# Kernel tuning notes

Measured on AMD Instinct MI355X. Metric: run time of the kernel, lower is better.

The kernel has to match this reference:

```python
import jax, jax.numpy as jnp
from jax import lax
import numpy as np

BNF = float((1.0 + 1e-5) ** -0.5)  # eval-mode BatchNorm with fresh init (mean=0,var=1,gamma=1,beta=0)
DN = ('NCHW', 'OIHW', 'NCHW')


def conv(x, w, b, stride=1, pad=1):
    y = lax.conv_general_dilated(x, w, (stride, stride), [(pad, pad), (pad, pad)], dimension_numbers=DN)
    return y + b[None, :, None, None]


def conv_t(x, w, b, stride=2, pad=1):
    # w in PyTorch ConvTranspose2d layout [Cin, Cout, kh, kw]
    wf = jnp.flip(w, (2, 3)).transpose(1, 0, 2, 3)  # -> [Cout, Cin, kh, kw]
    p = w.shape[2] - 1 - pad
    y = lax.conv_general_dilated(x, wf, (1, 1), [(p, p), (p, p)], lhs_dilation=(stride, stride), dimension_numbers=DN)
    return y + b[None, :, None, None]


def res_block(x, c1w, c1b, c2w, c2b, scw, scb, stride):
    sc = conv(x, scw, scb, stride, 0) * BNF
    h = jax.nn.relu(conv(x, c1w, c1b, stride, 1) * BNF)
    h = conv(h, c2w, c2b, 1, 1) * BNF
    return jax.nn.relu(h + sc)


def setup_inputs() -> dict:
    key = jax.random.key(0)
    ks = jax.random.split(key, 32)
    s = 0.05
    d = {}
    d['x'] = jax.random.normal(ks[0], (4, 1, 320, 320), jnp.float32)
    # encoder (scale_idx=3, scale_channels=512, embedding_dim=256)
    d['w0'] = jax.random.normal(ks[1], (128, 1, 3, 3)) * s;   d['b0'] = jnp.zeros((128,))
    d['a_c1w'] = jax.random.normal(ks[2], (256, 128, 3, 3)) * s; d['a_c1b'] = jnp.zeros((256,))
    d['a_c2w'] = jax.random.normal(ks[3], (256, 256, 3, 3)) * s; d['a_c2b'] = jnp.zeros((256,))
    d['a_scw'] = jax.random.normal(ks[4], (256, 128, 1, 1)) * s; d['a_scb'] = jnp.zeros((256,))
    d['b_c1w'] = jax.random.normal(ks[5], (512, 256, 3, 3)) * s; d['b_c1b'] = jnp.zeros((512,))
    d['b_c2w'] = jax.random.normal(ks[6], (512, 512, 3, 3)) * s; d['b_c2b'] = jnp.zeros((512,))
    d['b_scw'] = jax.random.normal(ks[7], (512, 256, 1, 1)) * s; d['b_scb'] = jnp.zeros((512,))
    d['ew'] = jax.random.normal(ks[8], (256, 512, 1, 1)) * s;    d['eb'] = jnp.zeros((256,))
    # codebook: uniform(-1/K, 1/K)
    d['codebook'] = jax.random.uniform(ks[9], (1024, 256), jnp.float32, -1.0 / 1024, 1.0 / 1024)
    # decoder
    d['d0w'] = jax.random.normal(ks[10], (512, 256, 1, 1)) * s;  d['d0b'] = jnp.zeros((512,))
    d['dt1w'] = jax.random.normal(ks[11], (512, 256, 4, 4)) * s; d['dt1b'] = jnp.zeros((256,))
    d['dt2w'] = jax.random.normal(ks[12], (256, 128, 4, 4)) * s; d['dt2b'] = jnp.zeros((128,))
    d['dow'] = jax.random.normal(ks[13], (1, 128, 3, 3)) * s;    d['dob'] = jnp.zeros((1,))
    return d


def reference(x, w0, b0, a_c1w, a_c1b, a_c2w, a_c2b, a_scw, a_scb,
              b_c1w, b_c1b, b_c2w, b_c2b, b_scw, b_scb, ew, eb, codebook,
              d0w, d0b, dt1w, dt1b, dt2w, dt2b, dow, dob):
    B = x.shape[0]
    # ---- encoder ----
    h = jax.nn.relu(conv(x, w0, b0, 1, 1) * BNF)                      # [B,128,320,320]
    h = res_block(h, a_c1w, a_c1b, a_c2w, a_c2b, a_scw, a_scb, 2)     # [B,256,160,160]
    h = res_block(h, b_c1w, b_c1b, b_c2w, b_c2b, b_scw, b_scb, 2)     # [B,512,80,80]
    z = conv(h, ew, eb, 1, 0) * BNF                                   # [B,256,80,80]
    # ---- vector quantize (faithful: flatten NCHW directly, D == embedding_dim) ----
    D = codebook.shape[1]
    flat = z.reshape(-1, D)                                           # [B*H*W, 256]
    dist = (jnp.sum(flat * flat, 1, keepdims=True)
            + jnp.sum(codebook * codebook, 1)
            - 2.0 * flat @ codebook.T)                                # [N, 1024]
    idx = jnp.argmin(dist, axis=1)                                    # [N]
    quant = codebook[idx].reshape(z.shape)
    zq = z + lax.stop_gradient(quant - z)                             # straight-through
    indices = idx.reshape(B, z.shape[2], z.shape[3]).astype(jnp.int32)
    # ---- decoder ----
    g = jax.nn.relu(conv(zq, d0w, d0b, 1, 0) * BNF)                   # [B,512,80,80]
    g = jax.nn.relu(conv_t(g, dt1w, dt1b) * BNF)                      # [B,256,160,160]
    g = jax.nn.relu(conv_t(g, dt2w, dt2b) * BNF)                      # [B,128,320,320]
    recon = jax.nn.sigmoid(conv(g, dow, dob, 1, 1))                   # [B,1,320,320]
    return recon, zq, indices
```

## Files before the change

### kernel.cpp

```cpp
#include <hip/hip_runtime.h>
#include <hip/hip_bf16.h>
#include <math.h>


static constexpr float kBNF = 0.9999950000374997f;

typedef short short8 __attribute__((ext_vector_type(8)));
typedef _Float16 half8 __attribute__((ext_vector_type(8)));
typedef float f32x4 __attribute__((ext_vector_type(4)));

__global__ __launch_bounds__(320) void conv0_k(const float* __restrict__ x,
                                               const float* __restrict__ w,
                                               const float* __restrict__ b,
                                               float* __restrict__ out) {
  const int H = 320, W = 320, OC = 128;
  int oy = blockIdx.x;
  int tx = threadIdx.x;
  __shared__ float in_s[3][W + 2];
  __shared__ float w_s[128 * 9];
  __shared__ float b_s[128];
  for (int e = tx; e < 3 * (W + 2); e += 320) {
    int r = e / (W + 2), c = e % (W + 2);
    int iy = oy + r - 1, ix = c - 1;
    float v = 0.f;
    if (iy >= 0 && iy < H && ix >= 0 && ix < W) v = x[iy * W + ix];
    in_s[r][c] = v;
  }
  for (int e = tx; e < 128 * 9; e += 320) w_s[e] = w[e];
  for (int e = tx; e < 128; e += 320) b_s[e] = b[e];
  __syncthreads();
  float iv[9];
#pragma unroll
  for (int r = 0; r < 3; ++r)
#pragma unroll
    for (int c = 0; c < 3; ++c) iv[r * 3 + c] = in_s[r][tx + c];
  for (int oc = 0; oc < OC; ++oc) {
    float acc = 0.f;
#pragma unroll
    for (int t = 0; t < 9; ++t) acc = fmaf(w_s[oc * 9 + t], iv[t], acc);
    float v32 = __fadd_rn(acc, b_s[oc]);
    v32 = __fmul_rn(v32, kBNF);
    out[(oc * H + oy) * W + tx] = fmaxf(v32, 0.f);
  }
}

__global__ __launch_bounds__(256) void prep_w3h_k(const float* __restrict__ w,
                                                  _Float16* __restrict__ wh,
                                                  int IC, int OC) {
  int i = blockIdx.x * 256 + threadIdx.x;
  int total = 2 * 9 * IC * OC;
  if (i >= total) return;
  int e = i & 7;
  int lane = (i >> 3) & 63;
  int rest = i >> 9;
  int ktiles = IC >> 5;
  int kT = rest % ktiles;
  int rest2 = rest / ktiles;
  int OCt = OC >> 4;
  int ocT = rest2 % OCt;
  int rest3 = rest2 / OCt;
  int tap = rest3 % 9;
  int split = rest3 / 9;
  int m = lane & 15, k = ((lane >> 4) << 3) + e;
  int oc = ocT * 16 + m, ic = kT * 32 + k;
  float v = w[((size_t)oc * IC + ic) * 9 + tap];
  _Float16 hi = (_Float16)v;
  wh[i] = (split == 0) ? hi : (_Float16)(v - (float)hi);
}

__global__ __launch_bounds__(256) void conv3s1_mfma_k(
    const float* __restrict__ in, const _Float16* __restrict__ wh,
    const float* __restrict__ bias, const float* __restrict__ skip,
    float* __restrict__ out, int IC, int HW_, int OC) {
  __shared__ __align__(16) _Float16 ldsH[3 * 20 * 40];
  __shared__ __align__(16) _Float16 ldsL[3 * 20 * 40];
  int t = threadIdx.x;
  int wv = t >> 6, l = t & 63;
  int px0 = blockIdx.x * 16;
  int oy = blockIdx.y;
  int ocT = blockIdx.z * 4 + wv;
  const int ktiles = IC >> 5;
  const int OCt = OC >> 4;
  int n = l & 15, koff = (l >> 4) * 8;
  f32x4 acc = {0.f, 0.f, 0.f, 0.f};
  const half8* wh8 = reinterpret_cast<const half8*>(wh);
  for (int kT = 0; kT < ktiles; ++kT) {
    __syncthreads();
    for (int e = t; e < 1728; e += 256) {
      int xi = e % 18;
      int rem = e / 18;
      int ic = rem & 31, r = rem >> 5;
      int iy = oy - 1 + r;
      int ix = px0 - 1 + xi;
      float v = 0.f;
      if (iy >= 0 && iy < HW_ && ix >= 0 && ix < HW_)
        v = in[((size_t)(kT * 32 + ic) * HW_ + iy) * HW_ + ix];
      _Float16 hi = (_Float16)v;
      ldsH[(r * 20 + xi) * 40 + ic] = hi;
      ldsL[(r * 20 + xi) * 40 + ic] = (_Float16)(v - (float)hi);
    }
    __syncthreads();
#pragma unroll
    for (int ky = 0; ky < 3; ++ky) {
#pragma unroll
      for (int kx = 0; kx < 3; ++kx) {
        int tap = ky * 3 + kx;
        half8 AH = wh8[(((tap)*OCt + ocT) * ktiles + kT) * 64 + l];
        half8 AL = wh8[(((9 + tap) * OCt + ocT) * ktiles + kT) * 64 + l];
        half8 BH = *reinterpret_cast<const half8*>(&ldsH[(ky * 20 + n + kx) * 40 + koff]);
        half8 BL = *reinterpret_cast<const half8*>(&ldsL[(ky * 20 + n + kx) * 40 + koff]);
        acc = __builtin_amdgcn_mfma_f32_16x16x32_f16(AH, BH, acc, 0, 0, 0);
        acc = __builtin_amdgcn_mfma_f32_16x16x32_f16(AH, BL, acc, 0, 0, 0);
        acc = __builtin_amdgcn_mfma_f32_16x16x32_f16(AL, BH, acc, 0, 0, 0);
      }
    }
  }
  int oc0 = ocT * 16 + ((l >> 4) << 2);
  int ox = px0 + n;
#pragma unroll
  for (int r = 0; r < 4; ++r) {
    int oc = oc0 + r;
    float bv = bias[oc];
    size_t idx = ((size_t)oc * HW_ + oy) * HW_ + ox;
    float v32 = __fadd_rn(acc[r], bv);
    v32 = __fmul_rn(v32, kBNF);
    v32 = __fadd_rn(v32, skip[idx]);
    out[idx] = fmaxf(v32, 0.f);
  }
}

__global__ __launch_bounds__(256) void conv3s2_mfma_k(
    const float* __restrict__ in, const _Float16* __restrict__ wh,
    const float* __restrict__ bias, float* __restrict__ out,
    int IC, int IH, int IW, int OC, int OH, int OW) {
  __shared__ __align__(16) _Float16 ldsEH[3 * 17 * 40];
  __shared__ __align__(16) _Float16 ldsEL[3 * 17 * 40];
  __shared__ __align__(16) _Float16 ldsOH[3 * 16 * 40];
  __shared__ __align__(16) _Float16 ldsOL[3 * 16 * 40];
  int t = threadIdx.x;
  int wv = t >> 6, l = t & 63;
  int px0 = blockIdx.x * 16;
  int oy = blockIdx.y;
  int ocT = blockIdx.z * 4 + wv;
  const int ktiles = IC >> 5;
  const int OCt = OC >> 4;
  int n = l & 15, koff = (l >> 4) * 8;
  f32x4 acc = {0.f, 0.f, 0.f, 0.f};
  const half8* wh8 = reinterpret_cast<const half8*>(wh);
  for (int kT = 0; kT < ktiles; ++kT) {
    __syncthreads();
    for (int e = t; e < 3168; e += 256) {
      int ic = e & 31;
      int rem = e >> 5;
      int xi = rem % 33, ky = rem / 33;
      int iy = oy * 2 - 1 + ky;
      int ix = px0 * 2 - 1 + xi;
      float v = 0.f;
      if (iy >= 0 && iy < IH && ix >= 0 && ix < IW)
        v = in[((size_t)(kT * 32 + ic) * IH + iy) * IW + ix];
      _Float16 hi = (_Float16)v;
      _Float16 lo = (_Float16)(v - (float)hi);
      int hrow = xi >> 1;
      if (xi & 1) {
        ldsOH[(ky * 16 + hrow) * 40 + ic] = hi;
        ldsOL[(ky * 16 + hrow) * 40 + ic] = lo;
      } else {
        ldsEH[(ky * 17 + hrow) * 40 + ic] = hi;
        ldsEL[(ky * 17 + hrow) * 40 + ic] = lo;
      }
    }
    __syncthreads();
#pragma unroll
    for (int ky = 0; ky < 3; ++ky) {
#pragma unroll
      for (int kx = 0; kx < 3; ++kx) {
        int tap = ky * 3 + kx;
        half8 AH = wh8[(((tap)*OCt + ocT) * ktiles + kT) * 64 + l];
        half8 AL = wh8[(((9 + tap) * OCt + ocT) * ktiles + kT) * 64 + l];
        half8 BH, BL;
        if (kx == 0) {
          BH = *reinterpret_cast<const half8*>(&ldsEH[(ky * 17 + n) * 40 + koff]);
          BL = *reinterpret_cast<const half8*>(&ldsEL[(ky * 17 + n) * 40 + koff]);
        } else if (kx == 1) {
          BH = *reinterpret_cast<const half8*>(&ldsOH[(ky * 16 + n) * 40 + koff]);
          BL = *reinterpret_cast<const half8*>(&ldsOL[(ky * 16 + n) * 40 + koff]);
        } else {
          BH = *reinterpret_cast<const half8*>(&ldsEH[(ky * 17 + n + 1) * 40 + koff]);
          BL = *reinterpret_cast<const half8*>(&ldsEL[(ky * 17 + n + 1) * 40 + koff]);
        }
        acc = __builtin_amdgcn_mfma_f32_16x16x32_f16(AH, BH, acc, 0, 0, 0);
        acc = __builtin_amdgcn_mfma_f32_16x16x32_f16(AH, BL, acc, 0, 0, 0);
        acc = __builtin_amdgcn_mfma_f32_16x16x32_f16(AL, BH, acc, 0, 0, 0);
      }
    }
  }
  int oc0 = ocT * 16 + ((l >> 4) << 2);
  int ox = px0 + n;
#pragma unroll
  for (int r = 0; r < 4; ++r) {
    int oc = oc0 + r;
    float bv = bias[oc];
    size_t idx = ((size_t)oc * OH + oy) * OW + ox;
    float v32 = __fadd_rn(acc[r], bv);
    v32 = __fmul_rn(v32, kBNF);
    out[idx] = fmaxf(v32, 0.f);
  }
}

template <int S, bool RELU>
__global__ __launch_bounds__(256) void conv1x1_k(
    const float* __restrict__ in, const float* __restrict__ w,
    const float* __restrict__ bias, float* __restrict__ out,
    int IC, int IH, int IW, int OC, int OH, int OW) {
  __shared__ float in_s[16][64];
  __shared__ float w_s[16][64];
  const int P = OH * OW;
  int t = threadIdx.x;
  int p0 = blockIdx.x * 64;
  int oc0 = blockIdx.y * 64;
  int oc4 = (t >> 4) * 4, px4 = (t & 15) * 4;
  float acc[4][4] = {};
  for (int ic0 = 0; ic0 < IC; ic0 += 16) {
    __syncthreads();
    {
      int e = t;
#pragma unroll
      for (int k = 0; k < 4; ++k, e += 256) {
        int icr = e >> 6, pxr = e & 63;
        int p = p0 + pxr;
        float v = 0.f;
        if (p < P) {
          int oy = p / OW, ox = p % OW;
          v = in[((ic0 + icr) * IH + oy * S) * IW + ox * S];
        }
        in_s[icr][pxr] = v;
      }
      e = t;
#pragma unroll
      for (int k = 0; k < 4; ++k, e += 256) {
        int icr = e >> 6, ocr = e & 63;
        w_s[icr][ocr] = w[(oc0 + ocr) * IC + ic0 + icr];
      }
    }
    __syncthreads();
#pragma unroll
    for (int icr = 0; icr < 16; ++icr) {
      float4 iv = *reinterpret_cast<const float4*>(&in_s[icr][px4]);
      float4 wv = *reinterpret_cast<const float4*>(&w_s[icr][oc4]);
      const float* ip = (const float*)&iv;
      const float* wp = (const float*)&wv;
#pragma unroll
      for (int o = 0; o < 4; ++o)
#pragma unroll
        for (int p = 0; p < 4; ++p)
          acc[o][p] = fmaf(wp[o], ip[p], acc[o][p]);
    }
  }
  int p = p0 + px4;
  if (p < P) {
    int oy = p / OW, ox = p % OW;
#pragma unroll
    for (int o = 0; o < 4; ++o) {
      int oc = oc0 + oc4 + o;
      float bv = bias[oc];
      float4 rv;
      float* rp = (float*)&rv;
#pragma unroll
      for (int pp = 0; pp < 4; ++pp) {
        float v32 = __fadd_rn(acc[o][pp], bv);
        v32 = __fmul_rn(v32, kBNF);
        if (RELU) v32 = fmaxf(v32, 0.f);
        rp[pp] = v32;
      }
      *reinterpret_cast<float4*>(&out[((size_t)oc * OH + oy) * OW + ox]) = rv;
    }
  }
}

__global__ __launch_bounds__(256) void prep_wb_k(const float* __restrict__ w,
                                                 __hip_bfloat16* __restrict__ wb,
                                                 int IC, int OC) {
  int i = blockIdx.x * 256 + threadIdx.x;
  int total = 16 * IC * OC;
  if (i >= total) return;
  int per_cfg = IC * OC;
  int cfg = i / per_cfg;
  int r = i - cfg * per_cfg;
  int ktiles = IC >> 5;
  int ocT = r / (ktiles * 512);
  int r2 = r - ocT * (ktiles * 512);
  int kT = r2 >> 9;
  int f = r2 & 511;
  int lane = f >> 3, e = f & 7;
  int m = lane & 15, kk = ((lane >> 4) << 3) + e;
  int oc = ocT * 16 + m, ic = kT * 32 + kk;
  int kyb = cfg >> 3, ty = (cfg >> 2) & 1, kx = cfg & 3;
  int ky = kyb + 2 * ty;
  wb[i] = __float2bfloat16(w[((size_t)ic * OC + oc) * 16 + ky * 4 + kx]);
}

__global__ __launch_bounds__(256) void convt_mfma_k(
    const float* __restrict__ in, const __hip_bfloat16* __restrict__ wb,
    const float* __restrict__ bias, float* __restrict__ out,
    int IC, int IH, int IW, int OC, int OH, int OW) {
  __shared__ __align__(16) __hip_bfloat16 lds[2 * 18 * 40];
  int t = threadIdx.x;
  int wv = t >> 6, l = t & 63;
  int ox0 = blockIdx.x * 32;
  int oy = blockIdx.y;
  int oc0w = blockIdx.z * 64 + wv * 16;
  int kyb = (oy & 1) ? 0 : 1;
  int hb = ox0 >> 1;
  int iy0n = oy + 1 - kyb;
  int iy0 = iy0n >> 1;
  bool ok0 = (iy0 < IH);
  int iy1n = oy + 1 - kyb - 2;
  int iy1 = iy1n >> 1;
  bool ok1 = (iy1n >= 0) && (iy1 < IH);
  f32x4 accE = {0.f, 0.f, 0.f, 0.f};
  f32x4 accO = {0.f, 0.f, 0.f, 0.f};
  const int ktiles = IC >> 5;
  int n = l & 15, koff = (l >> 4) * 8;
  const short8* wb8 = reinterpret_cast<const short8*>(wb);
  int ocT = oc0w >> 4;
  const int OCt = OC >> 4;
  for (int kT = 0; kT < ktiles; ++kT) {
    __syncthreads();
    for (int e = t; e < 1152; e += 256) {
      int ic = e / 36;
      int r = e - ic * 36;
      int ty = r / 18, xi = r - ty * 18;
      int ix = hb - 1 + xi;
      int iy = ty ? iy1 : iy0;
      bool ok = ty ? ok1 : ok0;
      float v = 0.f;
      if (ok && ix >= 0 && ix < IW)
        v = in[((size_t)(kT * 32 + ic) * IH + iy) * IW + ix];
      lds[(ty * 18 + xi) * 40 + ic] = __float2bfloat16(v);
    }
    __syncthreads();
#pragma unroll
    for (int ty = 0; ty < 2; ++ty) {
      short8 A0 = wb8[((((kyb * 2 + ty) * 4 + 0) * OCt + ocT) * ktiles + kT) * 64 + l];
      short8 A1 = wb8[((((kyb * 2 + ty) * 4 + 1) * OCt + ocT) * ktiles + kT) * 64 + l];
      short8 A2 = wb8[((((kyb * 2 + ty) * 4 + 2) * OCt + ocT) * ktiles + kT) * 64 + l];
      short8 A3 = wb8[((((kyb * 2 + ty) * 4 + 3) * OCt + ocT) * ktiles + kT) * 64 + l];
      short8 b0 = *reinterpret_cast<const short8*>(&lds[(ty * 18 + 0 + n) * 40 + koff]);
      short8 b1 = *reinterpret_cast<const short8*>(&lds[(ty * 18 + 1 + n) * 40 + koff]);
      short8 b2 = *reinterpret_cast<const short8*>(&lds[(ty * 18 + 2 + n) * 40 + koff]);
      accE = __builtin_amdgcn_mfma_f32_16x16x32_bf16(A1, b1, accE, 0, 0, 0);
      accE = __builtin_amdgcn_mfma_f32_16x16x32_bf16(A3, b0, accE, 0, 0, 0);
      accO = __builtin_amdgcn_mfma_f32_16x16x32_bf16(A0, b2, accO, 0, 0, 0);
      accO = __builtin_amdgcn_mfma_f32_16x16x32_bf16(A2, b1, accO, 0, 0, 0);
    }
  }
  int ocr0 = oc0w + ((l >> 4) << 2);
  int oxE = ox0 + 2 * n;
  int oxO = ox0 + 1 + 2 * n;
#pragma unroll
  for (int r = 0; r < 4; ++r) {
    float bv = bias[ocr0 + r];
    size_t rowbase = ((size_t)(ocr0 + r) * OH + oy) * OW;
    out[rowbase + oxE] = fmaxf((accE[r] + bv) * kBNF, 0.f);
    out[rowbase + oxO] = fmaxf((accO[r] + bv) * kBNF, 0.f);
  }
}

__global__ __launch_bounds__(320) void dow_k(const float* __restrict__ in,
                                             const float* __restrict__ w,
                                             const float* __restrict__ bias,
                                             float* __restrict__ out) {
  const int H = 320, W = 320, IC = 128;
  int oy = blockIdx.x;
  int tx = threadIdx.x;
  __shared__ float in_s[4][3][W + 2];
  __shared__ float w_s[IC * 9];
  for (int e = tx; e < IC * 9; e += 320) w_s[e] = w[e];
  float acc = 0.f;
  for (int ic0 = 0; ic0 < IC; ic0 += 4) {
    __syncthreads();
    for (int e = tx; e < 4 * 3 * (W + 2); e += 320) {
      int icr = e / (3 * (W + 2));
      int rem = e - icr * (3 * (W + 2));
      int r = rem / (W + 2), c = rem - r * (W + 2);
      int iy = oy + r - 1, ix = c - 1;
      float v = 0.f;
      if (iy >= 0 && iy < H && ix >= 0 && ix < W)
        v = in[((ic0 + icr) * H + iy) * W + ix];
      in_s[icr][r][c] = v;
    }
    __syncthreads();
#pragma unroll
    for (int icr = 0; icr < 4; ++icr)
#pragma unroll
      for (int r = 0; r < 3; ++r)
#pragma unroll
        for (int c = 0; c < 3; ++c)
          acc = fmaf(w_s[(ic0 + icr) * 9 + r * 3 + c], in_s[icr][r][tx + c], acc);
  }
  acc += bias[0];
  out[oy * W + tx] = 1.f / (1.f + expf(-acc));
}

__global__ __launch_bounds__(256) void cbprep_np(const float* __restrict__ cb,
                                                 float* __restrict__ c2f) {
  int e = blockIdx.x, t = threadIdx.x;
  __shared__ float a[256];
  a[t] = cb[e * 256 + t];
  __syncthreads();
  if (t == 0) {
    float tot = 0.f;
    for (int h = 0; h < 2; ++h) {
      const float* p = a + h * 128;
      float r[8];
#pragma unroll
      for (int j = 0; j < 8; ++j) r[j] = __fmul_rn(p[j], p[j]);
      for (int i = 8; i < 128; i += 8)
#pragma unroll
        for (int j = 0; j < 8; ++j) r[j] = __fadd_rn(r[j], __fmul_rn(p[i + j], p[i + j]));
      float s = __fadd_rn(__fadd_rn(__fadd_rn(r[0], r[1]), __fadd_rn(r[2], r[3])),
                          __fadd_rn(__fadd_rn(r[4], r[5]), __fadd_rn(r[6], r[7])));
      tot = (h == 0) ? s : __fadd_rn(tot, s);
    }
    c2f[e] = tot;
  }
}

__global__ __launch_bounds__(256) void vq_ref_k(const float* __restrict__ z,
                                                const float* __restrict__ cb,
                                                const float* __restrict__ c2f,
                                                float* __restrict__ zq_out,
                                                float* __restrict__ idx_out) {
  int n0 = blockIdx.x * 4;
  int t = threadIdx.x;
  __shared__ float f[4][256];
  __shared__ float dist[4][1024];
  __shared__ float rr[4][2][8];
  __shared__ float f2s[4];
  __shared__ int bestIdx[4];
  for (int e = t; e < 1024; e += 256) {
    int r = e >> 8, c = e & 255;
    f[r][c] = z[(size_t)(n0 + r) * 256 + c];
  }
  __syncthreads();
  if (t < 64) {
    int row = t >> 4, hh = (t >> 3) & 1, j = t & 7;
    const float* p = f[row] + hh * 128;
    float r = __fmul_rn(p[j], p[j]);
    for (int i = 8; i < 128; i += 8) r = __fadd_rn(r, __fmul_rn(p[i + j], p[i + j]));
    rr[row][hh][j] = r;
  }
  __syncthreads();
  if (t < 4) {
    float s0 = __fadd_rn(__fadd_rn(__fadd_rn(rr[t][0][0], rr[t][0][1]), __fadd_rn(rr[t][0][2], rr[t][0][3])),
                         __fadd_rn(__fadd_rn(rr[t][0][4], rr[t][0][5]), __fadd_rn(rr[t][0][6], rr[t][0][7])));
    float s1 = __fadd_rn(__fadd_rn(__fadd_rn(rr[t][1][0], rr[t][1][1]), __fadd_rn(rr[t][1][2], rr[t][1][3])),
                         __fadd_rn(__fadd_rn(rr[t][1][4], rr[t][1][5]), __fadd_rn(rr[t][1][6], rr[t][1][7])));
    f2s[t] = __fadd_rn(s0, s1);
  }
  __syncthreads();
  for (int e = t; e < 1024; e += 256) {
    const float4* cbe = reinterpret_cast<const float4*>(cb + (size_t)e * 256);
    double d0 = 0.0, d1 = 0.0, d2 = 0.0, d3 = 0.0;
    for (int d = 0; d < 64; ++d) {
      float4 c4 = cbe[d];
      float4 f0 = *reinterpret_cast<const float4*>(&f[0][d * 4]);
      float4 f1 = *reinterpret_cast<const float4*>(&f[1][d * 4]);
      float4 f2v = *reinterpret_cast<const float4*>(&f[2][d * 4]);
      float4 f3 = *reinterpret_cast<const float4*>(&f[3][d * 4]);
      d0 = fma((double)f0.x, (double)c4.x, d0); d0 = fma((double)f0.y, (double)c4.y, d0);
      d0 = fma((double)f0.z, (double)c4.z, d0); d0 = fma((double)f0.w, (double)c4.w, d0);
      d1 = fma((double)f1.x, (double)c4.x, d1); d1 = fma((double)f1.y, (double)c4.y, d1);
      d1 = fma((double)f1.z, (double)c4.z, d1); d1 = fma((double)f1.w, (double)c4.w, d1);
      d2 = fma((double)f2v.x, (double)c4.x, d2); d2 = fma((double)f2v.y, (double)c4.y, d2);
      d2 = fma((double)f2v.z, (double)c4.z, d2); d2 = fma((double)f2v.w, (double)c4.w, d2);
      d3 = fma((double)f3.x, (double)c4.x, d3); d3 = fma((double)f3.y, (double)c4.y, d3);
      d3 = fma((double)f3.z, (double)c4.z, d3); d3 = fma((double)f3.w, (double)c4.w, d3);
    }
    float c2e = c2f[e];
    dist[0][e] = __fsub_rn(__fadd_rn(f2s[0], c2e), __fmul_rn(2.f, (float)d0));
    dist[1][e] = __fsub_rn(__fadd_rn(f2s[1], c2e), __fmul_rn(2.f, (float)d1));
    dist[2][e] = __fsub_rn(__fadd_rn(f2s[2], c2e), __fmul_rn(2.f, (float)d2));
    dist[3][e] = __fsub_rn(__fadd_rn(f2s[3], c2e), __fmul_rn(2.f, (float)d3));
  }
  __syncthreads();
  {
    int row = t >> 6, l = t & 63;
    float bv = dist[row][l];
    int bi = l;
    for (int e = l + 64; e < 1024; e += 64) {
      float v = dist[row][e];
      if (v < bv) { bv = v; bi = e; }
    }
#pragma unroll
    for (int m = 1; m < 64; m <<= 1) {
      float ov = __shfl_xor(bv, m, 64);
      int oi = __shfl_xor(bi, m, 64);
      if (ov < bv || (ov == bv && oi < bi)) { bv = ov; bi = oi; }
    }
    if (l == 0) {
      bestIdx[row] = bi;
      idx_out[n0 + row] = (float)bi;
    }
  }
  __syncthreads();
#pragma unroll
  for (int r = 0; r < 4; ++r)
    zq_out[(size_t)(n0 + r) * 256 + t] = cb[(size_t)bestIdx[r] * 256 + t];
}

extern "C" void kernel_launch(void* const* d_in, const int* in_sizes, int n_in,
                              void* d_out, int out_size, void* d_ws, size_t ws_size,
                              hipStream_t stream) {
  const float* x = (const float*)d_in[0];
  const float* w0 = (const float*)d_in[1];
  const float* b0 = (const float*)d_in[2];
  const float* a_c1w = (const float*)d_in[3];
  const float* a_c1b = (const float*)d_in[4];
  const float* a_c2w = (const float*)d_in[5];
  const float* a_c2b = (const float*)d_in[6];
  const float* a_scw = (const float*)d_in[7];
  const float* a_scb = (const float*)d_in[8];
  const float* b_c1w = (const float*)d_in[9];
  const float* b_c1b = (const float*)d_in[10];
  const float* b_c2w = (const float*)d_in[11];
  const float* b_c2b = (const float*)d_in[12];
  const float* b_scw = (const float*)d_in[13];
  const float* b_scb = (const float*)d_in[14];
  const float* ew = (const float*)d_in[15];
  const float* eb = (const float*)d_in[16];
  const float* cb = (const float*)d_in[17];
  const float* d0w = (const float*)d_in[18];
  const float* d0b = (const float*)d_in[19];
  const float* dt1w = (const float*)d_in[20];
  const float* dt1b = (const float*)d_in[21];
  const float* dt2w = (const float*)d_in[22];
  const float* dt2b = (const float*)d_in[23];
  const float* doww = (const float*)d_in[24];
  const float* dob = (const float*)d_in[25];

  float* ws = (float*)d_ws;
  float* A = ws;
  float* Bf = ws + 13107200;
  float* Cf = ws + 19660800;
  float* c2f = ws + 26214400;
  _Float16* wh_ac1 = (_Float16*)(void*)Cf;
  _Float16* wh_bc1 = (_Float16*)(void*)(Bf + 3300000);
  _Float16* wh_ac2 = (_Float16*)(void*)(A + 6600000);
  _Float16* wh_bc2 = (_Float16*)(void*)(A + 3300000);
  __hip_bfloat16* wb_dt1 = (__hip_bfloat16*)(void*)A;
  __hip_bfloat16* wb_dt2 = (__hip_bfloat16*)(void*)(Bf + 3400000);

  float* outf = (float*)d_out;
  float* recon = outf;
  float* zq = outf + 409600;
  float* idxo = zq + 6553600;

  cbprep_np<<<1024, 256, 0, stream>>>(cb, c2f);

  for (int b = 0; b < 4; ++b) {
    const float* xb = x + (size_t)b * 102400;
    float* zqb = zq + (size_t)b * 1638400;
    float* idxb = idxo + (size_t)b * 6400;
    float* reconb = recon + (size_t)b * 102400;

    conv0_k<<<320, 320, 0, stream>>>(xb, w0, b0, A);
    prep_w3h_k<<<2304, 256, 0, stream>>>(a_c1w, wh_ac1, 128, 256);
    conv3s2_mfma_k<<<dim3(10, 160, 4), 256, 0, stream>>>(
        A, wh_ac1, a_c1b, Bf, 128, 320, 320, 256, 160, 160);
    conv1x1_k<2, false><<<dim3(400, 4), 256, 0, stream>>>(
        A, a_scw, a_scb, Cf, 128, 320, 320, 256, 160, 160);
    prep_w3h_k<<<4608, 256, 0, stream>>>(a_c2w, wh_ac2, 256, 256);
    conv3s1_mfma_k<<<dim3(10, 160, 4), 256, 0, stream>>>(
        Bf, wh_ac2, a_c2b, Cf, A, 256, 160, 256);
    prep_w3h_k<<<9216, 256, 0, stream>>>(b_c1w, wh_bc1, 256, 512);
    conv3s2_mfma_k<<<dim3(5, 80, 8), 256, 0, stream>>>(
        A, wh_bc1, b_c1b, Bf, 256, 160, 160, 512, 80, 80);
    conv1x1_k<2, false><<<dim3(100, 8), 256, 0, stream>>>(
        A, b_scw, b_scb, Cf, 256, 160, 160, 512, 80, 80);
    prep_w3h_k<<<18432, 256, 0, stream>>>(b_c2w, wh_bc2, 512, 512);
    conv3s1_mfma_k<<<dim3(5, 80, 8), 256, 0, stream>>>(
        Bf, wh_bc2, b_c2b, Cf, A, 512, 80, 512);
    conv1x1_k<1, false><<<dim3(100, 4), 256, 0, stream>>>(
        A, ew, eb, Cf, 512, 80, 80, 256, 80, 80);
    vq_ref_k<<<1600, 256, 0, stream>>>(Cf, cb, c2f, zqb, idxb);
    prep_wb_k<<<8192, 256, 0, stream>>>(dt1w, wb_dt1, 512, 256);
    prep_wb_k<<<2048, 256, 0, stream>>>(dt2w, wb_dt2, 256, 128);
    conv1x1_k<1, true><<<dim3(100, 8), 256, 0, stream>>>(
        zqb, d0w, d0b, Bf, 256, 80, 80, 512, 80, 80);
    convt_mfma_k<<<dim3(5, 160, 4), 256, 0, stream>>>(
        Bf, wb_dt1, dt1b, Cf, 512, 80, 80, 256, 160, 160);
    convt_mfma_k<<<dim3(10, 320, 2), 256, 0, stream>>>(
        Cf, wb_dt2, dt2b, A, 256, 160, 160, 128, 320, 320);
    dow_k<<<320, 320, 0, stream>>>(A, doww, dob, reconb);
  }
}
```

Before: 6.907 ms.

## Compute four output-channel tiles per wave in encoder 3x3 MFMA convs

Templates the stride-1 and stride-2 3x3 MFMA conv kernels on NOC so each wave accumulates four 16-channel output tiles. Each B fragment read from LDS is reused across four accumulators, and the grid z-dimension shrinks by four, so the split-fp16 input staging into LDS happens a quarter as often. The cost is more accumulator and weight registers per wave and fewer blocks, which can lower occupancy, especially for the 80x80 layers that now launch only 800 blocks.

```diff
diff --git a/kernel.cpp b/kernel.cpp
--- a/kernel.cpp
+++ b/kernel.cpp
@@ -68,6 +68,7 @@
   wh[i] = (split == 0) ? hi : (_Float16)(v - (float)hi);
 }
 
+template <int NOC>
 __global__ __launch_bounds__(256) void conv3s1_mfma_k(
     const float* __restrict__ in, const _Float16* __restrict__ wh,
     const float* __restrict__ bias, const float* __restrict__ skip,
@@ -78,11 +79,13 @@
   int wv = t >> 6, l = t & 63;
   int px0 = blockIdx.x * 16;
   int oy = blockIdx.y;
-  int ocT = blockIdx.z * 4 + wv;
+  int ocT0 = (blockIdx.z * 4 + wv) * NOC;
   const int ktiles = IC >> 5;
   const int OCt = OC >> 4;
   int n = l & 15, koff = (l >> 4) * 8;
-  f32x4 acc = {0.f, 0.f, 0.f, 0.f};
+  f32x4 acc[NOC];
+#pragma unroll
+  for (int j = 0; j < NOC; ++j) acc[j] = {0.f, 0.f, 0.f, 0.f};
   const half8* wh8 = reinterpret_cast<const half8*>(wh);
   for (int kT = 0; kT < ktiles; ++kT) {
     __syncthreads();
@@ -105,30 +108,37 @@
 #pragma unroll
       for (int kx = 0; kx < 3; ++kx) {
         int tap = ky * 3 + kx;
-        half8 AH = wh8[(((tap)*OCt + ocT) * ktiles + kT) * 64 + l];
-        half8 AL = wh8[(((9 + tap) * OCt + ocT) * ktiles + kT) * 64 + l];
         half8 BH = *reinterpret_cast<const half8*>(&ldsH[(ky * 20 + n + kx) * 40 + koff]);
         half8 BL = *reinterpret_cast<const half8*>(&ldsL[(ky * 20 + n + kx) * 40 + koff]);
-        acc = __builtin_amdgcn_mfma_f32_16x16x32_f16(AH, BH, acc, 0, 0, 0);
-        acc = __builtin_amdgcn_mfma_f32_16x16x32_f16(AH, BL, acc, 0, 0, 0);
-        acc = __builtin_amdgcn_mfma_f32_16x16x32_f16(AL, BH, acc, 0, 0, 0);
+#pragma unroll
+        for (int j = 0; j < NOC; ++j) {
+          half8 AH = wh8[(((tap)*OCt + (ocT0 + j)) * ktiles + kT) * 64 + l];
+          half8 AL = wh8[(((9 + tap) * OCt + (ocT0 + j)) * ktiles + kT) * 64 + l];
+          acc[j] = __builtin_amdgcn_mfma_f32_16x16x32_f16(AH, BH, acc[j], 0, 0, 0);
+          acc[j] = __builtin_amdgcn_mfma_f32_16x16x32_f16(AH, BL, acc[j], 0, 0, 0);
+          acc[j] = __builtin_amdgcn_mfma_f32_16x16x32_f16(AL, BH, acc[j], 0, 0, 0);
+        }
       }
     }
   }
-  int oc0 = ocT * 16 + ((l >> 4) << 2);
   int ox = px0 + n;
 #pragma unroll
-  for (int r = 0; r < 4; ++r) {
-    int oc = oc0 + r;
-    float bv = bias[oc];
-    size_t idx = ((size_t)oc * HW_ + oy) * HW_ + ox;
-    float v32 = __fadd_rn(acc[r], bv);
-    v32 = __fmul_rn(v32, kBNF);
-    v32 = __fadd_rn(v32, skip[idx]);
-    out[idx] = fmaxf(v32, 0.f);
-  }
-}
-
+  for (int j = 0; j < NOC; ++j) {
+    int oc0 = (ocT0 + j) * 16 + ((l >> 4) << 2);
+#pragma unroll
+    for (int r = 0; r < 4; ++r) {
+      int oc = oc0 + r;
+      float bv = bias[oc];
+      size_t idx = ((size_t)oc * HW_ + oy) * HW_ + ox;
+      float v32 = __fadd_rn(acc[j][r], bv);
+      v32 = __fmul_rn(v32, kBNF);
+      v32 = __fadd_rn(v32, skip[idx]);
+      out[idx] = fmaxf(v32, 0.f);
+    }
+  }
+}
+
+template <int NOC>
 __global__ __launch_bounds__(256) void conv3s2_mfma_k(
     const float* __restrict__ in, const _Float16* __restrict__ wh,
     const float* __restrict__ bias, float* __restrict__ out,
@@ -141,11 +151,13 @@
   int wv = t >> 6, l = t & 63;
   int px0 = blockIdx.x * 16;
   int oy = blockIdx.y;
-  int ocT = blockIdx.z * 4 + wv;
+  int ocT0 = (blockIdx.z * 4 + wv) * NOC;
   const int ktiles = IC >> 5;
   const int OCt = OC >> 4;
   int n = l & 15, koff = (l >> 4) * 8;
-  f32x4 acc = {0.f, 0.f, 0.f, 0.f};
+  f32x4 acc[NOC];
+#pragma unroll
+  for (int j = 0; j < NOC; ++j) acc[j] = {0.f, 0.f, 0.f, 0.f};
   const half8* wh8 = reinterpret_cast<const half8*>(wh);
   for (int kT = 0; kT < ktiles; ++kT) {
     __syncthreads();
@@ -175,8 +187,6 @@
 #pragma unroll
       for (int kx = 0; kx < 3; ++kx) {
         int tap = ky * 3 + kx;
-        half8 AH = wh8[(((tap)*OCt + ocT) * ktiles + kT) * 64 + l];
-        half8 AL = wh8[(((9 + tap) * OCt + ocT) * ktiles + kT) * 64 + l];
         half8 BH, BL;
         if (kx == 0) {
           BH = *reinterpret_cast<const half8*>(&ldsEH[(ky * 17 + n) * 40 + koff]);
@@ -188,22 +198,30 @@
           BH = *reinterpret_cast<const half8*>(&ldsEH[(ky * 17 + n + 1) * 40 + koff]);
           BL = *reinterpret_cast<const half8*>(&ldsEL[(ky * 17 + n + 1) * 40 + koff]);
         }
-        acc = __builtin_amdgcn_mfma_f32_16x16x32_f16(AH, BH, acc, 0, 0, 0);
-        acc = __builtin_amdgcn_mfma_f32_16x16x32_f16(AH, BL, acc, 0, 0, 0);
-        acc = __builtin_amdgcn_mfma_f32_16x16x32_f16(AL, BH, acc, 0, 0, 0);
+#pragma unroll
+        for (int j = 0; j < NOC; ++j) {
+          half8 AH = wh8[(((tap)*OCt + (ocT0 + j)) * ktiles + kT) * 64 + l];
+          half8 AL = wh8[(((9 + tap) * OCt + (ocT0 + j)) * ktiles + kT) * 64 + l];
+          acc[j] = __builtin_amdgcn_mfma_f32_16x16x32_f16(AH, BH, acc[j], 0, 0, 0);
+          acc[j] = __builtin_amdgcn_mfma_f32_16x16x32_f16(AH, BL, acc[j], 0, 0, 0);
+          acc[j] = __builtin_amdgcn_mfma_f32_16x16x32_f16(AL, BH, acc[j], 0, 0, 0);
+        }
       }
     }
   }
-  int oc0 = ocT * 16 + ((l >> 4) << 2);
   int ox = px0 + n;
 #pragma unroll
-  for (int r = 0; r < 4; ++r) {
-    int oc = oc0 + r;
-    float bv = bias[oc];
-    size_t idx = ((size_t)oc * OH + oy) * OW + ox;
-    float v32 = __fadd_rn(acc[r], bv);
-    v32 = __fmul_rn(v32, kBNF);
-    out[idx] = fmaxf(v32, 0.f);
+  for (int j = 0; j < NOC; ++j) {
+    int oc0 = (ocT0 + j) * 16 + ((l >> 4) << 2);
+#pragma unroll
+    for (int r = 0; r < 4; ++r) {
+      int oc = oc0 + r;
+      float bv = bias[oc];
+      size_t idx = ((size_t)oc * OH + oy) * OW + ox;
+      float v32 = __fadd_rn(acc[j][r], bv);
+      v32 = __fmul_rn(v32, kBNF);
+      out[idx] = fmaxf(v32, 0.f);
+    }
   }
 }
 
@@ -566,20 +584,20 @@
 
     conv0_k<<<320, 320, 0, stream>>>(xb, w0, b0, A);
     prep_w3h_k<<<2304, 256, 0, stream>>>(a_c1w, wh_ac1, 128, 256);
-    conv3s2_mfma_k<<<dim3(10, 160, 4), 256, 0, stream>>>(
+    conv3s2_mfma_k<4><<<dim3(10, 160, 1), 256, 0, stream>>>(
         A, wh_ac1, a_c1b, Bf, 128, 320, 320, 256, 160, 160);
     conv1x1_k<2, false><<<dim3(400, 4), 256, 0, stream>>>(
         A, a_scw, a_scb, Cf, 128, 320, 320, 256, 160, 160);
     prep_w3h_k<<<4608, 256, 0, stream>>>(a_c2w, wh_ac2, 256, 256);
-    conv3s1_mfma_k<<<dim3(10, 160, 4), 256, 0, stream>>>(
+    conv3s1_mfma_k<4><<<dim3(10, 160, 1), 256, 0, stream>>>(
         Bf, wh_ac2, a_c2b, Cf, A, 256, 160, 256);
     prep_w3h_k<<<9216, 256, 0, stream>>>(b_c1w, wh_bc1, 256, 512);
-    conv3s2_mfma_k<<<dim3(5, 80, 8), 256, 0, stream>>>(
+    conv3s2_mfma_k<4><<<dim3(5, 80, 2), 256, 0, stream>>>(
         A, wh_bc1, b_c1b, Bf, 256, 160, 160, 512, 80, 80);
     conv1x1_k<2, false><<<dim3(100, 8), 256, 0, stream>>>(
         A, b_scw, b_scb, Cf, 256, 160, 160, 512, 80, 80);
     prep_w3h_k<<<18432, 256, 0, stream>>>(b_c2w, wh_bc2, 512, 512);
-    conv3s1_mfma_k<<<dim3(5, 80, 8), 256, 0, stream>>>(
+    conv3s1_mfma_k<4><<<dim3(5, 80, 2), 256, 0, stream>>>(
         Bf, wh_bc2, b_c2b, Cf, A, 512, 80, 512);
     conv1x1_k<1, false><<<dim3(100, 4), 256, 0, stream>>>(
         A, ew, eb, Cf, 512, 80, 80, 256, 80, 80);
```

Measured after the change: 8.287 ms. 1.2x slower.
